# Kernel optimization log

Measured on AMD Instinct MI355X. Metric: run time of the kernel, lower is better.

The kernel has to match this reference:

```python
import jax
import jax.numpy as jnp
from jax import lax
import numpy as np

IN_CH, HID, GROUPS = 1024, 256, 8
B, H, W = 16, 64, 64
CPG = HID // GROUPS  # channels per group = 32
EPS = 1e-5


def setup_inputs() -> dict:
    key = jax.random.key(0)
    ks = jax.random.split(key, 8)
    s = 0.02  # small init scale so activations stay well-behaved
    return {
        "x": jax.random.normal(ks[0], (B, IN_CH, H, W), jnp.float32),
        "ctx_w": jax.random.normal(ks[1], (HID, IN_CH), jnp.float32) * s,
        "ctx_b": jnp.zeros((HID,), jnp.float32),
        "kg_w1": jax.random.normal(ks[2], (2 * HID, HID), jnp.float32) * s,
        "kg_b1": jnp.zeros((2 * HID,), jnp.float32),
        "kg_w2": jax.random.normal(ks[3], (GROUPS * 9, 2 * HID), jnp.float32) * s,
        "kg_b2": jnp.zeros((GROUPS * 9,), jnp.float32),
        "in_w": jax.random.normal(ks[4], (HID, IN_CH), jnp.float32) * s,
        "in_b": jnp.zeros((HID,), jnp.float32),
        "out_w": jax.random.normal(ks[5], (HID, HID), jnp.float32) * s,
        "out_b": jnp.zeros((HID,), jnp.float32),
        "gamma": jnp.ones((HID,), jnp.float32),
        "beta": jnp.zeros((HID,), jnp.float32),
    }


def reference(x, ctx_w, ctx_b, kg_w1, kg_b1, kg_w2, kg_b2,
              in_w, in_b, out_w, out_b, gamma, beta):
    b = x.shape[0]
    # context pooling: global avg pool -> 1x1 conv -> relu
    ctx = jnp.mean(x, axis=(2, 3))                       # [B, C_in]
    ctx = jax.nn.relu(ctx @ ctx_w.T + ctx_b)             # [B, HID]
    # kernel generator MLP -> per-sample per-group 3x3 kernels
    hddn = jax.nn.relu(ctx @ kg_w1.T + kg_b1)            # [B, 2*HID]
    kernels = (hddn @ kg_w2.T + kg_b2).reshape(b, GROUPS, 3, 3)
    # input transform (1x1 conv)
    xt = jnp.einsum('bchw,oc->bohw', x, in_w) + in_b[None, :, None, None]
    # expand group kernels to per-channel depthwise kernels [B, HID, 3, 3]
    kch = jnp.repeat(kernels, CPG, axis=1)
    # per-sample depthwise 3x3 conv, padding=1
    def dwconv(xi, ki):  # xi: [HID, H, W], ki: [HID, 3, 3]
        return lax.conv_general_dilated(
            xi[None], ki[:, None], window_strides=(1, 1), padding='SAME',
            dimension_numbers=('NCHW', 'OIHW', 'NCHW'),
            feature_group_count=HID)[0]
    out = jax.vmap(dwconv)(xt, kch)                      # [B, HID, H, W]
    # output transform (1x1 conv)
    out = jnp.einsum('bchw,oc->bohw', out, out_w) + out_b[None, :, None, None]
    # BatchNorm2d (training-mode batch statistics)
    mean = jnp.mean(out, axis=(0, 2, 3))
    var = jnp.var(out, axis=(0, 2, 3))
    out = gamma[None, :, None, None] * (out - mean[None, :, None, None]) \
          * lax.rsqrt(var[None, :, None, None] + EPS) + beta[None, :, None, None]
    return xt + out
```

## Files before the change

### kernel.cpp

```cpp
#include <hip/hip_runtime.h>

#define BATCH 16
#define CIN   1024
#define HID   256
#define HW    4096

typedef __attribute__((ext_vector_type(8))) short bf16x8;
typedef __attribute__((ext_vector_type(4))) float f32x4;

struct __align__(16) f4  { float v[4]; };
struct __align__(8)  us4 { unsigned short v[4]; };
struct __align__(16) us8 { unsigned short v[8]; };

__device__ __forceinline__ float bf2f(unsigned short u) {
  unsigned int x = ((unsigned int)u) << 16;
  return __builtin_bit_cast(float, x);
}
__device__ __forceinline__ unsigned short f2bf(float f) {
  unsigned int u = __builtin_bit_cast(unsigned int, f);
  u += 0x7fff + ((u >> 16) & 1);
  return (unsigned short)(u >> 16);
}

#define LGWB() do { __builtin_amdgcn_sched_barrier(0); \
  asm volatile("s_waitcnt lgkmcnt(0)" ::: "memory"); \
  __builtin_amdgcn_s_barrier(); \
  __builtin_amdgcn_sched_barrier(0); } while (0)

__global__ __launch_bounds__(256)
void prep_kernel(const float* __restrict__ A1, unsigned short* __restrict__ O1,
                 const float* __restrict__ A2, unsigned short* __restrict__ O2,
                 float* __restrict__ zbuf)
{
  const int bidx = blockIdx.x;
  if (bidx >= 160) {
    int idx = (bidx - 160) * 256 + threadIdx.x;
    if (idx < 16896) zbuf[idx] = 0.f;
    return;
  }
  const float* A; unsigned short* O; int KD, u;
  if (bidx < 128) { A = A1; O = O1; KD = 1024; u = bidx * 256 + threadIdx.x; }
  else            { A = A2; O = O2; KD = 256;  u = (bidx - 128) * 256 + threadIdx.x; }
  const int t    = u >> 11;
  const int r    = u & 2047;
  const int wm   = r >> 9, kk = (r >> 8) & 1, mi = (r >> 6) & 3, lane = r & 63;
  const int row  = wm * 64 + mi * 16 + (lane & 15);
  const int k    = t * 64 + kk * 32 + (lane >> 4) * 8;
  f4 v0 = *(const f4*)(A + (size_t)row * KD + k);
  f4 v1 = *(const f4*)(A + (size_t)row * KD + k + 4);
  us8 w = { f2bf(v0.v[0]), f2bf(v0.v[1]), f2bf(v0.v[2]), f2bf(v0.v[3]),
            f2bf(v1.v[0]), f2bf(v1.v[1]), f2bf(v1.v[2]), f2bf(v1.v[3]) };
  *(us8*)(O + (size_t)u * 8) = w;
}

__global__ __launch_bounds__(512, 2)
void gemm1_kernel(const unsigned short* __restrict__ Afrag, const float* __restrict__ xb,
                  const float* __restrict__ bias, unsigned short* __restrict__ Cout,
                  float* __restrict__ ctx_sum)
{
  constexpr int NT = 16;
  __shared__ unsigned short B_sh[2][128 * 64];
  __shared__ float ctx_lds[1024];

  const int tid  = threadIdx.x;
  const int lane = tid & 63;
  const int wv   = tid >> 6;
  const int wm   = wv >> 1, wn = wv & 1;
  const int lr   = lane & 15, lg = lane >> 4;
  const int hi   = lane >> 5, q = lane & 31;

  const int b    = blockIdx.x >> 5;
  const int pix0 = (blockIdx.x & 31) << 7;

  for (int i = tid; i < 1024; i += 512) ctx_lds[i] = 0.f;
  __syncthreads();

  f32x4 acc[4][4] = {};
  const size_t rowbase = ((size_t)b * CIN + 8 * wv + hi) * HW + pix0 + 4 * q;
  const char*  abase   = (const char*)Afrag + wm * 8192 + lane * 16;

  bf16x8 aA[8], aB[8];
  f4 rfA[4], rfB[4];

  auto ISSUE_A = [&](int t, bf16x8* a) {
    const char* p = abase + t * 32768;
    #pragma unroll
    for (int i = 0; i < 8; ++i) a[i] = *(const bf16x8*)(p + i * 1024);
  };
  auto LOADB = [&](int t, f4* rf) {
    const float* p = xb + rowbase + (size_t)t * 64 * HW;
    #pragma unroll
    for (int i = 0; i < 4; ++i) rf[i] = *(const f4*)(p + (size_t)(2 * i) * HW);
  };
  auto WRITEB = [&](int sel, int t, f4* rf) {
    #pragma unroll
    for (int i = 0; i < 4; ++i) {
      float s = rf[i].v[0] + rf[i].v[1] + rf[i].v[2] + rf[i].v[3];
      #pragma unroll
      for (int m = 1; m < 32; m <<= 1) s += __shfl_xor(s, m, 64);
      if (q == 0) atomicAdd(&ctx_lds[t * 64 + 8 * wv + 2 * i + hi], s);
    }
    unsigned int u[4][2];
    #pragma unroll
    for (int i = 0; i < 4; ++i) {
      asm("v_cvt_pk_bf16_f32 %0, %1, %2" : "=v"(u[i][0]) : "v"(rf[i].v[0]), "v"(rf[i].v[1]));
      asm("v_cvt_pk_bf16_f32 %0, %1, %2" : "=v"(u[i][1]) : "v"(rf[i].v[2]), "v"(rf[i].v[3]));
    }
    unsigned int w[4][2];
    #pragma unroll
    for (int i = 0; i < 4; ++i) {
      w[i][0] = __shfl_xor(u[i][0], 32, 64);
      w[i][1] = __shfl_xor(u[i][1], 32, 64);
    }
    #pragma unroll
    for (int jj = 0; jj < 2; ++jj) {
      unsigned int A0 = hi ? w[2][jj] : u[0][jj];
      unsigned int A1 = hi ? u[2][jj] : w[0][jj];
      unsigned int A2 = hi ? w[3][jj] : u[1][jj];
      unsigned int A3 = hi ? u[3][jj] : w[1][jj];
      #pragma unroll
      for (int sub = 0; sub < 2; ++sub) {
        unsigned int lo, h2;
        if (sub == 0) { lo = (A0 & 0xffffu) | (A1 << 16);  h2 = (A2 & 0xffffu) | (A3 << 16); }
        else          { lo = (A0 >> 16) | (A1 & 0xffff0000u); h2 = (A2 >> 16) | (A3 & 0xffff0000u); }
        int p  = 4 * q + jj * 2 + sub;
        int fx = ((p >> 2) ^ p) & 7;
        int byte = p * 128 + (((wv ^ fx) & 7) << 4) + hi * 8;
        uint2 val; val.x = lo; val.y = h2;
        *(uint2*)((char*)B_sh[sel] + byte) = val;
      }
    }
  };
  auto COMPUTE = [&](int sel, bf16x8* a) {
    #pragma unroll
    for (int kk = 0; kk < 2; ++kk) {
      bf16x8 bfr[4];
      #pragma unroll
      for (int ni = 0; ni < 4; ++ni) {
        int pr = wn * 64 + ni * 16 + lr;
        int fx = ((pr >> 2) ^ pr) & 7;
        int byte = pr * 128 + ((((kk * 4 + lg) ^ fx) & 7) << 4);
        bfr[ni] = *(const bf16x8*)((const char*)B_sh[sel] + byte);
      }
      #pragma unroll
      for (int mi = 0; mi < 4; ++mi)
        #pragma unroll
        for (int ni = 0; ni < 4; ++ni)
          acc[mi][ni] = __builtin_amdgcn_mfma_f32_16x16x32_bf16(a[kk * 4 + mi], bfr[ni], acc[mi][ni], 0, 0, 0);
    }
  };

  ISSUE_A(0, aA);
  LOADB(0, rfA);
  LOADB(1, rfB);

  #pragma unroll
  for (int t = 0; t < NT; t += 2) {
    WRITEB(0, t, rfA);
    ISSUE_A(t + 1, aB);
    __builtin_amdgcn_sched_barrier(0);
    if (t + 2 < NT) LOADB(t + 2, rfA);
    LGWB();
    COMPUTE(0, aA);
    WRITEB(1, t + 1, rfB);
    if (t + 2 < NT) ISSUE_A(t + 2, aA);
    __builtin_amdgcn_sched_barrier(0);
    if (t + 3 < NT) LOADB(t + 3, rfB);
    LGWB();
    COMPUTE(1, aB);
  }

  #pragma unroll
  for (int mi = 0; mi < 4; ++mi) {
    #pragma unroll
    for (int r = 0; r < 4; ++r) {
      int o = wm * 64 + mi * 16 + lg * 4 + r;
      float bo = bias[o];
      #pragma unroll
      for (int ni = 0; ni < 4; ++ni) {
        int pix = pix0 + wn * 64 + ni * 16 + lr;
        Cout[((size_t)(b * HID + o)) * HW + pix] = f2bf(acc[mi][ni][r] + bo);
      }
    }
  }
  __syncthreads();
  for (int e = tid; e < 1024; e += 512)
    atomicAdd(&ctx_sum[(size_t)b * 1024 + e], ctx_lds[e]);
}

__global__ __launch_bounds__(512, 2)
void gemm2_fused_kernel(const unsigned short* __restrict__ Afrag,
                        const unsigned short* __restrict__ xt,
                        const float* __restrict__ kern, const float* __restrict__ bias,
                        unsigned short* __restrict__ Cout, float* __restrict__ bn_sums)
{
  constexpr int NT = 4;
  __shared__ unsigned short B_sh[128 * 64];
  __shared__ unsigned short xs[64 * 260];
  __shared__ float kf_s[72];
  __shared__ float bn_lds[512];

  const int tid  = threadIdx.x;
  const int lane = tid & 63;
  const int wv   = tid >> 6;
  const int wm   = wv >> 1, wn = wv & 1;
  const int lr   = lane & 15, lg = lane >> 4;

  const int b    = blockIdx.x >> 5;
  const int R    = blockIdx.x & 31;
  const int pix0 = R << 7;
  const int g0   = R << 1;

  if (tid < 512) bn_lds[tid] = 0.f;
  if (tid < 72)  kf_s[tid] = kern[b * 72 + tid];
  __syncthreads();

  f32x4 acc[4][4] = {};
  const int c4 = tid & 15, q = tid >> 4;
  const int prow  = q >> 4;
  const int pcol4 = (q & 15) << 2;
  const int grp9  = (c4 >> 3) * 9;

  const char* abase = (const char*)Afrag + wm * 8192 + lane * 16;

  bf16x8 aA[8];
  us8 rx[4];

  auto PREXS = [&](int t) {
    #pragma unroll
    for (int it = 0; it < 4; ++it) {
      int flat = it * 512 + tid;
      int ch = flat >> 5, r4 = (flat >> 3) & 3, c8 = flat & 7;
      int grow = g0 - 1 + r4;
      if ((unsigned)grow < 64u) {
        rx[it] = *(const us8*)(xt + ((size_t)(b * HID + t * 64 + ch) << 12) + grow * 64 + c8 * 8);
      } else {
        us8 z = {0, 0, 0, 0, 0, 0, 0, 0}; rx[it] = z;
      }
    }
  };
  auto WRXS = [&]() {
    #pragma unroll
    for (int it = 0; it < 4; ++it) {
      int flat = it * 512 + tid;
      int ch = flat >> 5, r4 = (flat >> 3) & 3, c8 = flat & 7;
      int o = ch * 260 + r4 * 64 + c8 * 8;
      *(us4*)(xs + o)     = *(const us4*)(&rx[it].v[0]);
      *(us4*)(xs + o + 4) = *(const us4*)(&rx[it].v[4]);
    }
  };
  auto ISSUE_A = [&](int t) {
    const char* p = abase + t * 32768;
    #pragma unroll
    for (int i = 0; i < 8; ++i) aA[i] = *(const bf16x8*)(p + i * 1024);
  };

  PREXS(0);
  ISSUE_A(0);

  for (int t = 0; t < NT; ++t) {
    WRXS();
    __syncthreads();
    if (t + 1 < NT) PREXS(t + 1);
    {
      const float k0 = kf_s[2 * t * 9 + grp9 + 0], k1 = kf_s[2 * t * 9 + grp9 + 1], k2 = kf_s[2 * t * 9 + grp9 + 2];
      const float k3 = kf_s[2 * t * 9 + grp9 + 3], k4 = kf_s[2 * t * 9 + grp9 + 4], k5 = kf_s[2 * t * 9 + grp9 + 5];
      const float k6 = kf_s[2 * t * 9 + grp9 + 6], k7 = kf_s[2 * t * 9 + grp9 + 7], k8 = kf_s[2 * t * 9 + grp9 + 8];
      float dwv[4][4];
      #pragma unroll
      for (int i = 0; i < 4; ++i) {
        int ch = 4 * c4 + i;
        #pragma unroll
        for (int j = 0; j < 4; ++j) dwv[i][j] = 0.f;
        #pragma unroll
        for (int ky = 0; ky < 3; ++ky) {
          int ro = ch * 260 + (prow + ky) * 64;
          float v[6];
          unsigned int p0 = (pcol4 > 0)  ? *(const unsigned int*)(xs + ro + pcol4 - 2) : 0u;
          unsigned int p1 = *(const unsigned int*)(xs + ro + pcol4);
          unsigned int p2 = *(const unsigned int*)(xs + ro + pcol4 + 2);
          unsigned int p3 = (pcol4 < 60) ? *(const unsigned int*)(xs + ro + pcol4 + 4) : 0u;
          v[0] = bf2f((unsigned short)(p0 >> 16));
          v[1] = bf2f((unsigned short)(p1 & 0xffff));
          v[2] = bf2f((unsigned short)(p1 >> 16));
          v[3] = bf2f((unsigned short)(p2 & 0xffff));
          v[4] = bf2f((unsigned short)(p2 >> 16));
          v[5] = bf2f((unsigned short)(p3 & 0xffff));
          float ka = (ky == 0) ? k0 : (ky == 1) ? k3 : k6;
          float kb = (ky == 0) ? k1 : (ky == 1) ? k4 : k7;
          float kc = (ky == 0) ? k2 : (ky == 1) ? k5 : k8;
          #pragma unroll
          for (int j = 0; j < 4; ++j)
            dwv[i][j] += v[j] * ka + v[j + 1] * kb + v[j + 2] * kc;
        }
      }
      #pragma unroll
      for (int j = 0; j < 4; ++j) {
        int pix = 4 * q + j;
        us4 w = { f2bf(dwv[0][j]), f2bf(dwv[1][j]), f2bf(dwv[2][j]), f2bf(dwv[3][j]) };
        *(us4*)((char*)B_sh + pix * 128 + ((8 * c4) ^ ((pix & 7) << 4))) = w;
      }
    }
    __syncthreads();
    #pragma unroll
    for (int kk = 0; kk < 2; ++kk) {
      bf16x8 bfr[4];
      #pragma unroll
      for (int ni = 0; ni < 4; ++ni) {
        int pr = wn * 64 + ni * 16 + lr;
        bfr[ni] = *(const bf16x8*)((const char*)B_sh + pr * 128 + ((((kk << 2) | lg) ^ (pr & 7)) << 4));
      }
      #pragma unroll
      for (int mi = 0; mi < 4; ++mi)
        #pragma unroll
        for (int ni = 0; ni < 4; ++ni)
          acc[mi][ni] = __builtin_amdgcn_mfma_f32_16x16x32_bf16(aA[kk * 4 + mi], bfr[ni], acc[mi][ni], 0, 0, 0);
    }
    if (t + 1 < NT) ISSUE_A(t + 1);
  }

  #pragma unroll
  for (int mi = 0; mi < 4; ++mi) {
    #pragma unroll
    for (int r = 0; r < 4; ++r) {
      int o = wm * 64 + mi * 16 + lg * 4 + r;
      float bo = bias[o];
      #pragma unroll
      for (int ni = 0; ni < 4; ++ni) {
        int pix = pix0 + wn * 64 + ni * 16 + lr;
        float val = acc[mi][ni][r] + bo;
        Cout[((size_t)(b * HID + o)) * HW + pix] = f2bf(val);
        float s = val, s2 = val * val;
        #pragma unroll
        for (int msk = 1; msk < 16; msk <<= 1) {
          s  += __shfl_xor(s,  msk, 64);
          s2 += __shfl_xor(s2, msk, 64);
        }
        if (lr == 0) { atomicAdd(&bn_lds[o], s); atomicAdd(&bn_lds[256 + o], s2); }
      }
    }
  }
  __syncthreads();
  if (tid < 512) atomicAdd(&bn_sums[tid], bn_lds[tid]);
}

template<int K, int N, bool RELU>
__global__ __launch_bounds__(256)
void fc_kernel(const float* __restrict__ in, const float* __restrict__ w,
               const float* __restrict__ bias, float* __restrict__ out, float scale)
{
  const int wid  = (blockIdx.x << 2) | (threadIdx.x >> 6);
  const int lane = threadIdx.x & 63;
  const int b = wid / N, o = wid - b * N;
  const float* ip = in + (size_t)b * K;
  const float* wp = w  + (size_t)o * K;
  float p = 0.f;
  #pragma unroll
  for (int k = 0; k < K / 64; ++k) p += ip[lane + k * 64] * wp[lane + k * 64];
  #pragma unroll
  for (int m = 1; m < 64; m <<= 1) p += __shfl_xor(p, m, 64);
  if (lane == 0) {
    float v = p * scale + bias[o];
    out[(size_t)b * N + o] = RELU ? fmaxf(v, 0.f) : v;
  }
}

__global__ __launch_bounds__(256)
void final_kernel(const unsigned short* __restrict__ xt, const unsigned short* __restrict__ ot,
                  const float* __restrict__ bn_sums, const float* __restrict__ gamma,
                  const float* __restrict__ beta, float* __restrict__ out)
{
  __shared__ float sc_s[256], sh_s[256];
  {
    int t = threadIdx.x;
    const float inv_n = 1.f / 65536.f;
    float m  = bn_sums[t] * inv_n;
    float v  = bn_sums[256 + t] * inv_n - m * m;
    float sc = gamma[t] * rsqrtf(v + 1e-5f);
    sc_s[t] = sc;
    sh_s[t] = beta[t] - m * sc;
  }
  __syncthreads();
  int g = blockIdx.x * 256 + threadIdx.x;
  const int stride = 4096 * 256;
  #pragma unroll
  for (int it = 0; it < 4; ++it, g += stride) {
    int o = (g >> 10) & 255;
    us4 a = ((const us4*)xt)[g];
    us4 c = ((const us4*)ot)[g];
    float s = sc_s[o], h = sh_s[o];
    f4 r;
    #pragma unroll
    for (int j = 0; j < 4; ++j) r.v[j] = bf2f(a.v[j]) + s * bf2f(c.v[j]) + h;
    *(f4*)(out + (size_t)g * 4) = r;
  }
}

extern "C" void kernel_launch(void* const* d_in, const int* in_sizes, int n_in,
                              void* d_out, int out_size, void* d_ws, size_t ws_size,
                              hipStream_t stream)
{
  const float* x     = (const float*)d_in[0];
  const float* ctx_w = (const float*)d_in[1];
  const float* ctx_b = (const float*)d_in[2];
  const float* kg_w1 = (const float*)d_in[3];
  const float* kg_b1 = (const float*)d_in[4];
  const float* kg_w2 = (const float*)d_in[5];
  const float* kg_b2 = (const float*)d_in[6];
  const float* in_w  = (const float*)d_in[7];
  const float* in_b  = (const float*)d_in[8];
  const float* out_w = (const float*)d_in[9];
  const float* out_b = (const float*)d_in[10];
  const float* gamma = (const float*)d_in[11];
  const float* beta  = (const float*)d_in[12];
  float* out = (float*)d_out;

  char* ws = (char*)d_ws;
  unsigned short* xt = (unsigned short*)ws;
  unsigned short* ot = (unsigned short*)(ws + 33554432);
  float* ctx_sum = (float*)(ws + 67108864);
  float* bn_sums = ctx_sum + 16384;
  float* kern    = bn_sums + 512;
  float* ctxbuf  = kern + 1152;
  float* hddnbuf = ctxbuf + 4096;
  unsigned short* afrag1 = (unsigned short*)(ws + 67108864 + 131072);
  unsigned short* afrag2 = (unsigned short*)(ws + 67108864 + 131072 + 524288);

  prep_kernel<<<226, 256, 0, stream>>>(in_w, afrag1, out_w, afrag2, ctx_sum);
  gemm1_kernel<<<512, 512, 0, stream>>>(afrag1, x, in_b, xt, ctx_sum);
  fc_kernel<1024, 256, true ><<<1024, 256, 0, stream>>>(ctx_sum, ctx_w, ctx_b, ctxbuf, 1.f / 4096.f);
  fc_kernel< 256, 512, true ><<<2048, 256, 0, stream>>>(ctxbuf,  kg_w1, kg_b1, hddnbuf, 1.f);
  fc_kernel< 512,  72, false><<< 288, 256, 0, stream>>>(hddnbuf, kg_w2, kg_b2, kern,    1.f);
  gemm2_fused_kernel<<<512, 512, 0, stream>>>(afrag2, xt, kern, out_b, ot, bn_sums);
  final_kernel<<<4096, 256, 0, stream>>>(xt, ot, bn_sums, gamma, beta, out);
}
```

Measured before the change: 185.5 us.

## Double K-tile depth in gemm1 and use DPP/swizzle reductions for ctx sums

The input-transform GEMM now processes 128 input channels per pipeline stage instead of 64. It halves the number of stages and LDS barriers and widens the LDS stores to 16 bytes with an extended swizzle. The A fragments are now held in a single register array, loaded just before each compute stage instead of prefetched a stage ahead, which may expose global load latency. The per-row context-sum reduction replaces shuffle-xor with DPP and ds_swizzle adds. The change raises register and LDS use and may lower occupancy under launch_bounds(512,2).

New measurement: 190.3 us. +2.6%, slower.

```diff
diff --git a/kernel.cpp b/kernel.cpp
--- a/kernel.cpp
+++ b/kernel.cpp
@@ -26,6 +26,20 @@
   asm volatile("s_waitcnt lgkmcnt(0)" ::: "memory"); \
   __builtin_amdgcn_s_barrier(); \
   __builtin_amdgcn_sched_barrier(0); } while (0)
+
+__device__ __forceinline__ float dppadd_x1(float s) {
+  int v = __builtin_amdgcn_mov_dpp(__builtin_bit_cast(int, s), 0xB1, 0xF, 0xF, true);
+  return s + __builtin_bit_cast(float, v);
+}
+__device__ __forceinline__ float dppadd_x2(float s) {
+  int v = __builtin_amdgcn_mov_dpp(__builtin_bit_cast(int, s), 0x4E, 0xF, 0xF, true);
+  return s + __builtin_bit_cast(float, v);
+}
+template<int OFF>
+__device__ __forceinline__ float swzadd(float s) {
+  int v = __builtin_amdgcn_ds_swizzle(__builtin_bit_cast(int, s), OFF);
+  return s + __builtin_bit_cast(float, v);
+}
 
 __global__ __launch_bounds__(256)
 void prep_kernel(const float* __restrict__ A1, unsigned short* __restrict__ O1,
@@ -58,8 +72,8 @@
                   const float* __restrict__ bias, unsigned short* __restrict__ Cout,
                   float* __restrict__ ctx_sum)
 {
-  constexpr int NT = 16;
-  __shared__ unsigned short B_sh[2][128 * 64];
+  constexpr int NT = 8;
+  __shared__ unsigned short B_sh[2][128 * 128];
   __shared__ float ctx_lds[1024];
 
   const int tid  = threadIdx.x;
@@ -76,98 +90,101 @@
   __syncthreads();
 
   f32x4 acc[4][4] = {};
-  const size_t rowbase = ((size_t)b * CIN + 8 * wv + hi) * HW + pix0 + 4 * q;
+  const size_t rowbase = ((size_t)b * CIN + 16 * wv + hi) * HW + pix0 + 4 * q;
   const char*  abase   = (const char*)Afrag + wm * 8192 + lane * 16;
 
-  bf16x8 aA[8], aB[8];
-  f4 rfA[4], rfB[4];
-
-  auto ISSUE_A = [&](int t, bf16x8* a) {
-    const char* p = abase + t * 32768;
-    #pragma unroll
-    for (int i = 0; i < 8; ++i) a[i] = *(const bf16x8*)(p + i * 1024);
+  bf16x8 aA[16];
+  f4 rfA[8], rfB[8];
+
+  auto ISSUE_A = [&](int t) {
+    const char* p = abase + t * 65536;
+    #pragma unroll
+    for (int i = 0; i < 16; ++i) aA[i] = *(const bf16x8*)(p + (i >> 3) * 32768 + (i & 7) * 1024);
   };
   auto LOADB = [&](int t, f4* rf) {
-    const float* p = xb + rowbase + (size_t)t * 64 * HW;
-    #pragma unroll
-    for (int i = 0; i < 4; ++i) rf[i] = *(const f4*)(p + (size_t)(2 * i) * HW);
+    const float* p = xb + rowbase + (size_t)(t * 128) * HW;
+    #pragma unroll
+    for (int i = 0; i < 8; ++i) rf[i] = *(const f4*)(p + (size_t)(2 * i) * HW);
   };
   auto WRITEB = [&](int sel, int t, f4* rf) {
     #pragma unroll
-    for (int i = 0; i < 4; ++i) {
+    for (int i = 0; i < 8; ++i) {
       float s = rf[i].v[0] + rf[i].v[1] + rf[i].v[2] + rf[i].v[3];
-      #pragma unroll
-      for (int m = 1; m < 32; m <<= 1) s += __shfl_xor(s, m, 64);
-      if (q == 0) atomicAdd(&ctx_lds[t * 64 + 8 * wv + 2 * i + hi], s);
-    }
-    unsigned int u[4][2];
-    #pragma unroll
-    for (int i = 0; i < 4; ++i) {
+      s = dppadd_x1(s); s = dppadd_x2(s);
+      s = swzadd<0x101F>(s); s = swzadd<0x201F>(s); s = swzadd<0x401F>(s);
+      if (q == 0) atomicAdd(&ctx_lds[t * 128 + 16 * wv + 2 * i + hi], s);
+    }
+    unsigned int u[8][2];
+    #pragma unroll
+    for (int i = 0; i < 8; ++i) {
       asm("v_cvt_pk_bf16_f32 %0, %1, %2" : "=v"(u[i][0]) : "v"(rf[i].v[0]), "v"(rf[i].v[1]));
       asm("v_cvt_pk_bf16_f32 %0, %1, %2" : "=v"(u[i][1]) : "v"(rf[i].v[2]), "v"(rf[i].v[3]));
     }
-    unsigned int w[4][2];
-    #pragma unroll
-    for (int i = 0; i < 4; ++i) {
+    unsigned int w[8][2];
+    #pragma unroll
+    for (int i = 0; i < 8; ++i) {
       w[i][0] = __shfl_xor(u[i][0], 32, 64);
       w[i][1] = __shfl_xor(u[i][1], 32, 64);
     }
+    const int slotbase = 2 * wv + hi;
     #pragma unroll
     for (int jj = 0; jj < 2; ++jj) {
-      unsigned int A0 = hi ? w[2][jj] : u[0][jj];
-      unsigned int A1 = hi ? u[2][jj] : w[0][jj];
-      unsigned int A2 = hi ? w[3][jj] : u[1][jj];
-      unsigned int A3 = hi ? u[3][jj] : w[1][jj];
       #pragma unroll
       for (int sub = 0; sub < 2; ++sub) {
-        unsigned int lo, h2;
-        if (sub == 0) { lo = (A0 & 0xffffu) | (A1 << 16);  h2 = (A2 & 0xffffu) | (A3 << 16); }
-        else          { lo = (A0 >> 16) | (A1 & 0xffff0000u); h2 = (A2 >> 16) | (A3 & 0xffff0000u); }
+        unsigned int d[4];
+        #pragma unroll
+        for (int g = 0; g < 4; ++g) {
+          unsigned int e = hi ? w[4 + g][jj] : u[g][jj];
+          unsigned int o = hi ? u[4 + g][jj] : w[g][jj];
+          unsigned int lo16 = sub ? (e >> 16) : (e & 0xffffu);
+          unsigned int hi16 = sub ? (o & 0xffff0000u) : (o << 16);
+          d[g] = lo16 | hi16;
+        }
         int p  = 4 * q + jj * 2 + sub;
         int fx = ((p >> 2) ^ p) & 7;
-        int byte = p * 128 + (((wv ^ fx) & 7) << 4) + hi * 8;
-        uint2 val; val.x = lo; val.y = h2;
-        *(uint2*)((char*)B_sh[sel] + byte) = val;
-      }
-    }
-  };
-  auto COMPUTE = [&](int sel, bf16x8* a) {
-    #pragma unroll
-    for (int kk = 0; kk < 2; ++kk) {
+        int slotS = ((slotbase ^ fx) & 7) | (slotbase & 8);
+        uint4 val; val.x = d[0]; val.y = d[1]; val.z = d[2]; val.w = d[3];
+        *(uint4*)((char*)B_sh[sel] + p * 256 + slotS * 16) = val;
+      }
+    }
+  };
+  auto COMPUTE = [&](int sel) {
+    #pragma unroll
+    for (int kk = 0; kk < 4; ++kk) {
       bf16x8 bfr[4];
       #pragma unroll
       for (int ni = 0; ni < 4; ++ni) {
         int pr = wn * 64 + ni * 16 + lr;
         int fx = ((pr >> 2) ^ pr) & 7;
-        int byte = pr * 128 + ((((kk * 4 + lg) ^ fx) & 7) << 4);
-        bfr[ni] = *(const bf16x8*)((const char*)B_sh[sel] + byte);
+        int slot = kk * 4 + lg;
+        int slotS = ((slot ^ fx) & 7) | (slot & 8);
+        bfr[ni] = *(const bf16x8*)((const char*)B_sh[sel] + pr * 256 + slotS * 16);
       }
       #pragma unroll
       for (int mi = 0; mi < 4; ++mi)
         #pragma unroll
         for (int ni = 0; ni < 4; ++ni)
-          acc[mi][ni] = __builtin_amdgcn_mfma_f32_16x16x32_bf16(a[kk * 4 + mi], bfr[ni], acc[mi][ni], 0, 0, 0);
-    }
-  };
-
-  ISSUE_A(0, aA);
+          acc[mi][ni] = __builtin_amdgcn_mfma_f32_16x16x32_bf16(aA[kk * 4 + mi], bfr[ni], acc[mi][ni], 0, 0, 0);
+    }
+  };
+
   LOADB(0, rfA);
   LOADB(1, rfB);
 
   #pragma unroll
   for (int t = 0; t < NT; t += 2) {
+    ISSUE_A(t);
     WRITEB(0, t, rfA);
-    ISSUE_A(t + 1, aB);
     __builtin_amdgcn_sched_barrier(0);
     if (t + 2 < NT) LOADB(t + 2, rfA);
     LGWB();
-    COMPUTE(0, aA);
+    COMPUTE(0);
+    ISSUE_A(t + 1);
     WRITEB(1, t + 1, rfB);
-    if (t + 2 < NT) ISSUE_A(t + 2, aA);
     __builtin_amdgcn_sched_barrier(0);
     if (t + 3 < NT) LOADB(t + 3, rfB);
     LGWB();
-    COMPUTE(1, aB);
+    COMPUTE(1);
   }
 
   #pragma unroll
```
